# Kernel tuning notes

Measured on AMD Instinct MI355X. Metric: run time of the kernel, lower is better.

Reference implementation:

```python
import jax, jax.numpy as jnp
import numpy as np

N_NODES = 40000
N_EDGES = 640000
IN, HID, OUT = 128, 128, 47


def setup_inputs() -> dict:
    key = jax.random.key(0)
    ks = jax.random.split(key, 12)
    def glorot(k, shape):
        fan = sum(shape)
        return jax.random.normal(k, shape, dtype=jnp.float32) * jnp.sqrt(2.0 / fan)
    return {
        "x": jax.random.normal(ks[0], (N_NODES, IN), dtype=jnp.float32),
        "src": jax.random.randint(ks[1], (N_EDGES,), 0, N_NODES),
        "dst": jax.random.randint(ks[2], (N_EDGES,), 0, N_NODES),
        "W_self0": glorot(ks[3], (IN, HID)),
        "W_neigh0": glorot(ks[4], (IN, HID)),
        "b0": jnp.zeros((HID,), dtype=jnp.float32),
        "W_self1": glorot(ks[5], (HID, HID)),
        "W_neigh1": glorot(ks[6], (HID, HID)),
        "b1": jnp.zeros((HID,), dtype=jnp.float32),
        "W_self2": glorot(ks[7], (HID, OUT)),
        "W_neigh2": glorot(ks[8], (HID, OUT)),
        "b2": jnp.zeros((OUT,), dtype=jnp.float32),
    }


def _sage_conv(h, src, dst, W_self, W_neigh, b):
    # DGL SAGEConv('mean'): mean of neighbor (src) feats scattered to dst,
    # then fc_neigh(h_neigh) + fc_self(h_self) + bias.
    n = h.shape[0]
    deg = jax.ops.segment_sum(jnp.ones_like(dst, dtype=h.dtype), dst, num_segments=n)
    agg = jax.ops.segment_sum(h[src], dst, num_segments=n)          # [N, d] gather + scatter-add
    h_neigh = agg / jnp.maximum(deg, 1.0)[:, None]                   # isolated nodes -> 0 (DGL behavior)
    return h @ W_self + h_neigh @ W_neigh + b


def reference(x, src, dst, W_self0, W_neigh0, b0, W_self1, W_neigh1, b1,
              W_self2, W_neigh2, b2):
    # Dropout is identity in eval mode; omitted here.
    h = _sage_conv(x, src, dst, W_self0, W_neigh0, b0)
    h = jax.nn.relu(h)
    h = _sage_conv(h, src, dst, W_self1, W_neigh1, b1)
    h = jax.nn.relu(h)
    h = _sage_conv(h, src, dst, W_self2, W_neigh2, b2)
    return h
```

## Files before the change

kernel.cpp:

```cpp
#include <hip/hip_runtime.h>
#include <hip/hip_bf16.h>

#define NN 40000
#define NE 640000
#define NB 157

typedef __attribute__((ext_vector_type(8))) short bf16x8;
typedef __attribute__((ext_vector_type(4))) float f32x4;

static __device__ __forceinline__ unsigned short f2b(float f) {
    unsigned b = __float_as_uint(f);
    return (unsigned short)((b + 0x7FFFu + ((b >> 16) & 1u)) >> 16);
}
static __device__ __forceinline__ float blo(unsigned v) { return __uint_as_float(v << 16); }
static __device__ __forceinline__ float bhi(unsigned v) { return __uint_as_float(v & 0xffff0000u); }

static __device__ __forceinline__ void acc8(float* a, uint4 v) {
    a[0] += blo(v.x); a[1] += bhi(v.x);
    a[2] += blo(v.y); a[3] += bhi(v.y);
    a[4] += blo(v.z); a[5] += bhi(v.z);
    a[6] += blo(v.w); a[7] += bhi(v.w);
}
static __device__ __forceinline__ void acc4(float* a, uint2 v) {
    a[0] += blo(v.x); a[1] += bhi(v.x);
    a[2] += blo(v.y); a[3] += bhi(v.y);
}


__global__ void count_deg_kernel(const int* __restrict__ dst, int* __restrict__ deg, int n) {
    int i = blockIdx.x * blockDim.x + threadIdx.x;
    if (i < n) atomicAdd(&deg[dst[i]], 1);
}

__global__ __launch_bounds__(256) void scan1_kernel(const int* __restrict__ deg,
                                                    int* __restrict__ bsum) {
    int i = blockIdx.x * 256 + threadIdx.x;
    int v = (i < NN) ? deg[i] : 0;
#pragma unroll
    for (int off = 1; off < 64; off <<= 1) v += __shfl_xor(v, off);
    __shared__ int ws4[4];
    if ((threadIdx.x & 63) == 0) ws4[threadIdx.x >> 6] = v;
    __syncthreads();
    if (threadIdx.x == 0) bsum[blockIdx.x] = ws4[0] + ws4[1] + ws4[2] + ws4[3];
}

__global__ void scan_top_kernel(const int* __restrict__ bsum, int* __restrict__ btop) {
    int lane = threadIdx.x;
    int run = 0;
    for (int base = 0; base < NB; base += 64) {
        int idx = base + lane;
        int v = (idx < NB) ? bsum[idx] : 0;
        int s = v;
#pragma unroll
        for (int off = 1; off < 64; off <<= 1) { int t = __shfl_up(s, off); if (lane >= off) s += t; }
        if (idx < NB) btop[idx] = run + s - v;
        run += __shfl(s, 63);
    }
}

__global__ __launch_bounds__(256) void scan2_kernel(const int* __restrict__ deg,
                                                    const int* __restrict__ btop,
                                                    int* __restrict__ row_ptr) {
    int b = blockIdx.x;
    int i = b * 256 + threadIdx.x;
    int lane = threadIdx.x & 63, wv = threadIdx.x >> 6;
    int v = (i < NN) ? deg[i] : 0;
    int s = v;
#pragma unroll
    for (int off = 1; off < 64; off <<= 1) { int t = __shfl_up(s, off); if (lane >= off) s += t; }
    __shared__ int wsum[4];
    if (lane == 63) wsum[wv] = s;
    __syncthreads();
    int add = btop[b];
    for (int w = 0; w < wv; ++w) add += wsum[w];
    if (i < NN) row_ptr[i] = add + s - v;
    if (i == NN - 1) row_ptr[NN] = add + s;
}

__global__ void fill_csr_kernel(const int* __restrict__ src, const int* __restrict__ dst,
                                const int* __restrict__ row_ptr, int* __restrict__ cursor,
                                int* __restrict__ csr, int n) {
    int i = blockIdx.x * blockDim.x + threadIdx.x;
    if (i < n) {
        int d = dst[i];
        int pos = row_ptr[d] + atomicAdd(&cursor[d], 1);
        csr[pos] = src[i];
    }
}


__global__ __launch_bounds__(256) void prep_kernel(
    const float* __restrict__ x,
    const float* __restrict__ Ws0, const float* __restrict__ Wn0,
    const float* __restrict__ Ws1, const float* __restrict__ Wn1,
    const float* __restrict__ Ws2, const float* __restrict__ Wn2,
    int* __restrict__ zero_base, unsigned short* __restrict__ X,
    unsigned short* __restrict__ Wt0, unsigned short* __restrict__ Wt1,
    unsigned short* __restrict__ Wt2s, unsigned short* __restrict__ Wt2n) {
    int b = blockIdx.x, tid = threadIdx.x;
    if (b < 79) {
        int i = (b * 256 + tid) * 4;
        if (i < 80000) *(int4*)(zero_base + i) = (int4){0, 0, 0, 0};
    } else if (b < 5079) {
        int i = (b - 79) * 256 + tid;
        int e = i << 2;
        float4 v = *(const float4*)(x + e);
        uint2 o;
        o.x = f2b(v.x) | ((unsigned)f2b(v.y) << 16);
        o.y = f2b(v.z) | ((unsigned)f2b(v.w) << 16);
        *(uint2*)(X + e) = o;
    } else {
        int i = (b - 5079) * 256 + tid;
        if (i < 65536) {
            int l = i >> 15, j = i & 32767;
            int n = j >> 8, k = j & 255;
            const float* Ws = l ? Ws1 : Ws0;
            const float* Wn = l ? Wn1 : Wn0;
            float v = (k < 128) ? Ws[k * 128 + n] : Wn[(k - 128) * 128 + n];
            (l ? Wt1 : Wt0)[n * 256 + k] = f2b(v);
        } else if (i < 65536 + 6144) {
            int j = i - 65536;
            int n = j >> 7, k = j & 127;
            float v = (n < 47) ? Ws2[k * 47 + n] : 0.f;
            Wt2s[n * 128 + k] = f2b(v);
        } else if (i < 65536 + 12288) {
            int j = i - 65536 - 6144;
            int n = j >> 7, k = j & 127;
            float v = (n < 47) ? Wn2[k * 47 + n] : 0.f;
            Wt2n[n * 128 + k] = f2b(v);
        }
    }
}


template <bool RELU>
__global__ __launch_bounds__(256) void sage_layer_kernel(
    const unsigned short* __restrict__ Hin,
    const int* __restrict__ csr, const int* __restrict__ row_ptr,
    const unsigned short* __restrict__ Wt, const float* __restrict__ bias,
    unsigned short* __restrict__ Hout) {
    __shared__ unsigned short agg_lds[64 * 128];

    int tid = threadIdx.x;
    int wv = tid >> 6, lane = tid & 63;
    int lr = lane & 15, lg = lane >> 4;
    int m0 = blockIdx.x * 64;

    bf16x8 bfr[2][8];
    float bs[2];
#pragma unroll
    for (int c = 0; c < 2; ++c) {
        int n = (wv * 2 + c) * 16 + lr;
#pragma unroll
        for (int kt = 0; kt < 8; ++kt)
            bfr[c][kt] = *(const bf16x8*)(Wt + (size_t)n * 256 + kt * 32 + lg * 8);
        bs[c] = bias[n];
    }

    int nb = m0 + wv * 16;
    int rp = row_ptr[nb + (lane & 31) % 17];
    rp = __shfl(rp, lane % 17);
    int rp17 = (lane < 17) ? row_ptr[nb + lane] : 0;
    for (int t = 0; t < 16; ++t) {
        int beg = __shfl(rp17, t), end = __shfl(rp17, t + 1);
        float a[8] = {};
        int j = beg + lg;
        for (; j + 12 < end; j += 16) {
            int s0 = csr[j], s1 = csr[j + 4], s2 = csr[j + 8], s3 = csr[j + 12];
            uint4 v0 = *(const uint4*)(Hin + (size_t)s0 * 128 + lr * 8);
            uint4 v1 = *(const uint4*)(Hin + (size_t)s1 * 128 + lr * 8);
            uint4 v2 = *(const uint4*)(Hin + (size_t)s2 * 128 + lr * 8);
            uint4 v3 = *(const uint4*)(Hin + (size_t)s3 * 128 + lr * 8);
            acc8(a, v0); acc8(a, v1); acc8(a, v2); acc8(a, v3);
        }
        for (; j < end; j += 4) {
            uint4 v = *(const uint4*)(Hin + (size_t)csr[j] * 128 + lr * 8);
            acc8(a, v);
        }
#pragma unroll
        for (int k = 0; k < 8; ++k) {
            a[k] += __shfl_xor(a[k], 16);
            a[k] += __shfl_xor(a[k], 32);
        }
        if (lg == 0) {
            float inv = 1.0f / fmaxf((float)(end - beg), 1.0f);
            uint4 o;
            o.x = f2b(a[0] * inv) | ((unsigned)f2b(a[1] * inv) << 16);
            o.y = f2b(a[2] * inv) | ((unsigned)f2b(a[3] * inv) << 16);
            o.z = f2b(a[4] * inv) | ((unsigned)f2b(a[5] * inv) << 16);
            o.w = f2b(a[6] * inv) | ((unsigned)f2b(a[7] * inv) << 16);
            int row = wv * 16 + t;
            int chunk = lr ^ (row & 15);
            *(uint4*)&agg_lds[row * 128 + chunk * 8] = o;
        }
    }
    __syncthreads();

    for (int tt = 0; tt < 4; ++tt) {
        int mr = tt * 16 + lr;
        bf16x8 afr[8];
#pragma unroll
        for (int kt = 0; kt < 4; ++kt)
            afr[kt] = *(const bf16x8*)(Hin + (size_t)(m0 + mr) * 128 + kt * 32 + lg * 8);
#pragma unroll
        for (int kt = 0; kt < 4; ++kt) {
            int chunk = (kt * 4 + lg) ^ (mr & 15);
            afr[4 + kt] = *(const bf16x8*)&agg_lds[mr * 128 + chunk * 8];
        }
        f32x4 acc[2];
#pragma unroll
        for (int c = 0; c < 2; ++c) acc[c] = (f32x4){0.f, 0.f, 0.f, 0.f};
#pragma unroll
        for (int kt = 0; kt < 8; ++kt)
#pragma unroll
            for (int c = 0; c < 2; ++c)
                acc[c] = __builtin_amdgcn_mfma_f32_16x16x32_bf16(afr[kt], bfr[c][kt], acc[c], 0, 0, 0);
#pragma unroll
        for (int c = 0; c < 2; ++c) {
            int n = (wv * 2 + c) * 16 + lr;
#pragma unroll
            for (int r = 0; r < 4; ++r) {
                int m = m0 + tt * 16 + lg * 4 + r;
                float v = acc[c][r] + bs[c];
                if (RELU) v = fmaxf(v, 0.f);
                Hout[(size_t)m * 128 + n] = f2b(v);
            }
        }
    }
}


__global__ __launch_bounds__(192) void dual_gemm_kernel(
    const unsigned short* __restrict__ H2,
    const unsigned short* __restrict__ Wt2s, const unsigned short* __restrict__ Wt2n,
    const float* __restrict__ b2,
    float* __restrict__ out, unsigned short* __restrict__ Hn) {
    int wv = threadIdx.x >> 6, lane = threadIdx.x & 63;
    int lr = lane & 15, lg = lane >> 4;

    bf16x8 bfr[2][4];
    float bs[2];
#pragma unroll
    for (int c = 0; c < 2; ++c) {
        int t = wv * 2 + c;
        bool is_s = t < 3;
        int n = (is_s ? t : t - 3) * 16 + lr;
        const unsigned short* W = is_s ? Wt2s : Wt2n;
#pragma unroll
        for (int kt = 0; kt < 4; ++kt)
            bfr[c][kt] = *(const bf16x8*)(W + (size_t)n * 128 + kt * 32 + lg * 8);
        bs[c] = (is_s && n < 47) ? b2[n] : 0.f;
    }

    for (int tt = 0; tt < 4; ++tt) {
        int m0 = blockIdx.x * 64 + tt * 16;
        bf16x8 afr[4];
#pragma unroll
        for (int kt = 0; kt < 4; ++kt)
            afr[kt] = *(const bf16x8*)(H2 + (size_t)(m0 + lr) * 128 + kt * 32 + lg * 8);
        f32x4 acc[2];
#pragma unroll
        for (int c = 0; c < 2; ++c) acc[c] = (f32x4){0.f, 0.f, 0.f, 0.f};
#pragma unroll
        for (int kt = 0; kt < 4; ++kt)
#pragma unroll
            for (int c = 0; c < 2; ++c)
                acc[c] = __builtin_amdgcn_mfma_f32_16x16x32_bf16(afr[kt], bfr[c][kt], acc[c], 0, 0, 0);
#pragma unroll
        for (int c = 0; c < 2; ++c) {
            int t = wv * 2 + c;
            bool is_s = t < 3;
            int n = (is_s ? t : t - 3) * 16 + lr;
#pragma unroll
            for (int r = 0; r < 4; ++r) {
                int m = m0 + lg * 4 + r;
                float v = acc[c][r] + bs[c];
                if (is_s) {
                    if (n < 47) out[(size_t)m * 47 + n] = v;
                } else {
                    Hn[(size_t)m * 48 + n] = f2b(v);
                }
            }
        }
    }
}


__global__ void aggregate_out_kernel(const unsigned short* __restrict__ Hn,
                                     const int* __restrict__ csr,
                                     const int* __restrict__ row_ptr,
                                     float* __restrict__ out) {
    int node = (blockIdx.x * blockDim.x + threadIdx.x) >> 6;
    int lane = threadIdx.x & 63;
    if (node >= NN) return;
    int eg = lane >> 4, lc = lane & 15;
    int beg = row_ptr[node], end = row_ptr[node + 1];
    float a[4] = {};
    int j = beg + eg;
    for (; j + 12 < end; j += 16) {
        int s0 = csr[j], s1 = csr[j + 4], s2 = csr[j + 8], s3 = csr[j + 12];
        uint2 v0 = *(const uint2*)(Hn + (size_t)s0 * 48 + lc * 4);
        uint2 v1 = *(const uint2*)(Hn + (size_t)s1 * 48 + lc * 4);
        uint2 v2 = *(const uint2*)(Hn + (size_t)s2 * 48 + lc * 4);
        uint2 v3 = *(const uint2*)(Hn + (size_t)s3 * 48 + lc * 4);
        acc4(a, v0); acc4(a, v1); acc4(a, v2); acc4(a, v3);
    }
    for (; j < end; j += 4) {
        uint2 v = *(const uint2*)(Hn + (size_t)csr[j] * 48 + lc * 4);
        acc4(a, v);
    }
#pragma unroll
    for (int k = 0; k < 4; ++k) {
        a[k] += __shfl_xor(a[k], 16);
        a[k] += __shfl_xor(a[k], 32);
    }
    if (eg == 0 && lc < 12) {
        float inv = 1.0f / fmaxf((float)(end - beg), 1.0f);
        int c0 = lc * 4;
#pragma unroll
        for (int r = 0; r < 4; ++r)
            if (c0 + r < 47) out[(size_t)node * 47 + c0 + r] += a[r] * inv;
    }
}


extern "C" void kernel_launch(void* const* d_in, const int* in_sizes, int n_in,
                              void* d_out, int out_size, void* d_ws, size_t ws_size,
                              hipStream_t stream) {
    const float* x   = (const float*)d_in[0];
    const int*   src = (const int*)d_in[1];
    const int*   dst = (const int*)d_in[2];
    const float* Ws0 = (const float*)d_in[3];
    const float* Wn0 = (const float*)d_in[4];
    const float* b0  = (const float*)d_in[5];
    const float* Ws1 = (const float*)d_in[6];
    const float* Wn1 = (const float*)d_in[7];
    const float* b1  = (const float*)d_in[8];
    const float* Ws2 = (const float*)d_in[9];
    const float* Wn2 = (const float*)d_in[10];
    const float* b2  = (const float*)d_in[11];
    float* out = (float*)d_out;

    int* wsI     = (int*)d_ws;
    int* deg     = wsI;
    int* cursor  = wsI + 40000;
    int* row_ptr = wsI + 80000;
    int* csr     = wsI + 120004;
    unsigned short* X   = (unsigned short*)(wsI + 760004);
    unsigned short* H1  = X + (size_t)NN * 128;
    unsigned short* H2  = X;
    unsigned short* Wt0 = H1 + (size_t)NN * 128;
    unsigned short* Wt1 = Wt0 + 128 * 256;
    unsigned short* Wt2s = Wt1 + 128 * 256;
    unsigned short* Wt2n = Wt2s + 48 * 128;
    unsigned short* Hn  = Wt2n + 48 * 128;
    int* bsum = (int*)(Hn + (size_t)NN * 48 + 64);
    int* btop = bsum + NB;

    prep_kernel<<<5383, 256, 0, stream>>>(x, Ws0, Wn0, Ws1, Wn1, Ws2, Wn2,
                                          deg, X, Wt0, Wt1, Wt2s, Wt2n);
    count_deg_kernel<<<2500, 256, 0, stream>>>(dst, deg, NE);
    scan1_kernel<<<NB, 256, 0, stream>>>(deg, bsum);
    scan_top_kernel<<<1, 64, 0, stream>>>(bsum, btop);
    scan2_kernel<<<NB, 256, 0, stream>>>(deg, btop, row_ptr);
    fill_csr_kernel<<<2500, 256, 0, stream>>>(src, dst, row_ptr, cursor, csr, NE);

    sage_layer_kernel<true><<<625, 256, 0, stream>>>(X, csr, row_ptr, Wt0, b0, H1);
    sage_layer_kernel<true><<<625, 256, 0, stream>>>(H1, csr, row_ptr, Wt1, b1, H2);
    dual_gemm_kernel<<<625, 192, 0, stream>>>(H2, Wt2s, Wt2n, b2, out, Hn);
    aggregate_out_kernel<<<10000, 256, 0, stream>>>(Hn, csr, row_ptr, out);
}
```

Baseline: 216.4 us.

## Shrink per-block node tile to raise block count in SAGE layer kernels

Each block of the fused aggregate+GEMM layer kernel now handles 16 nodes instead of 64, so the launch grows from 625 to 2500 blocks. LDS use drops and weight fragments are loaded inside the MFMA loop instead of being held in registers. This aims to improve occupancy and load balance on the irregular gather phase, which had only 625 blocks for the GPU's many CUs. The cost is more redundant weight loads per node. The last-layer dual GEMM tile is also halved to give 1250 blocks.

```diff
diff --git a/kernel.cpp b/kernel.cpp
--- a/kernel.cpp
+++ b/kernel.cpp
@@ -139,30 +139,17 @@
     const int* __restrict__ csr, const int* __restrict__ row_ptr,
     const unsigned short* __restrict__ Wt, const float* __restrict__ bias,
     unsigned short* __restrict__ Hout) {
-    __shared__ unsigned short agg_lds[64 * 128];
+    __shared__ unsigned short agg_lds[16 * 128];
 
     int tid = threadIdx.x;
     int wv = tid >> 6, lane = tid & 63;
     int lr = lane & 15, lg = lane >> 4;
-    int m0 = blockIdx.x * 64;
-
-    bf16x8 bfr[2][8];
-    float bs[2];
-#pragma unroll
-    for (int c = 0; c < 2; ++c) {
-        int n = (wv * 2 + c) * 16 + lr;
-#pragma unroll
-        for (int kt = 0; kt < 8; ++kt)
-            bfr[c][kt] = *(const bf16x8*)(Wt + (size_t)n * 256 + kt * 32 + lg * 8);
-        bs[c] = bias[n];
-    }
-
-    int nb = m0 + wv * 16;
-    int rp = row_ptr[nb + (lane & 31) % 17];
-    rp = __shfl(rp, lane % 17);
-    int rp17 = (lane < 17) ? row_ptr[nb + lane] : 0;
-    for (int t = 0; t < 16; ++t) {
-        int beg = __shfl(rp17, t), end = __shfl(rp17, t + 1);
+    int m0 = blockIdx.x * 16;
+
+    int nb = m0 + wv * 4;
+    int rp5 = (lane < 5) ? row_ptr[nb + lane] : 0;
+    for (int t = 0; t < 4; ++t) {
+        int beg = __shfl(rp5, t), end = __shfl(rp5, t + 1);
         float a[8] = {};
         int j = beg + lg;
         for (; j + 12 < end; j += 16) {
@@ -189,43 +176,44 @@
             o.y = f2b(a[2] * inv) | ((unsigned)f2b(a[3] * inv) << 16);
             o.z = f2b(a[4] * inv) | ((unsigned)f2b(a[5] * inv) << 16);
             o.w = f2b(a[6] * inv) | ((unsigned)f2b(a[7] * inv) << 16);
-            int row = wv * 16 + t;
-            int chunk = lr ^ (row & 15);
+            int row = wv * 4 + t;
+            int chunk = lr ^ row;
             *(uint4*)&agg_lds[row * 128 + chunk * 8] = o;
         }
     }
     __syncthreads();
 
-    for (int tt = 0; tt < 4; ++tt) {
-        int mr = tt * 16 + lr;
-        bf16x8 afr[8];
-#pragma unroll
-        for (int kt = 0; kt < 4; ++kt)
-            afr[kt] = *(const bf16x8*)(Hin + (size_t)(m0 + mr) * 128 + kt * 32 + lg * 8);
-#pragma unroll
-        for (int kt = 0; kt < 4; ++kt) {
-            int chunk = (kt * 4 + lg) ^ (mr & 15);
-            afr[4 + kt] = *(const bf16x8*)&agg_lds[mr * 128 + chunk * 8];
-        }
-        f32x4 acc[2];
-#pragma unroll
-        for (int c = 0; c < 2; ++c) acc[c] = (f32x4){0.f, 0.f, 0.f, 0.f};
-#pragma unroll
-        for (int kt = 0; kt < 8; ++kt)
-#pragma unroll
-            for (int c = 0; c < 2; ++c)
-                acc[c] = __builtin_amdgcn_mfma_f32_16x16x32_bf16(afr[kt], bfr[c][kt], acc[c], 0, 0, 0);
-#pragma unroll
-        for (int c = 0; c < 2; ++c) {
-            int n = (wv * 2 + c) * 16 + lr;
-#pragma unroll
-            for (int r = 0; r < 4; ++r) {
-                int m = m0 + tt * 16 + lg * 4 + r;
-                float v = acc[c][r] + bs[c];
-                if (RELU) v = fmaxf(v, 0.f);
-                Hout[(size_t)m * 128 + n] = f2b(v);
-            }
-        }
+    bf16x8 afr[8];
+#pragma unroll
+    for (int kt = 0; kt < 4; ++kt)
+        afr[kt] = *(const bf16x8*)(Hin + (size_t)(m0 + lr) * 128 + kt * 32 + lg * 8);
+#pragma unroll
+    for (int kt = 0; kt < 4; ++kt) {
+        int chunk = (kt * 4 + lg) ^ lr;
+        afr[4 + kt] = *(const bf16x8*)&agg_lds[lr * 128 + chunk * 8];
+    }
+
+    int n0 = (wv * 2) * 16 + lr;
+    int n1 = n0 + 16;
+    f32x4 acc0 = (f32x4){0.f, 0.f, 0.f, 0.f};
+    f32x4 acc1 = (f32x4){0.f, 0.f, 0.f, 0.f};
+#pragma unroll
+    for (int kt = 0; kt < 8; ++kt) {
+        bf16x8 b0 = *(const bf16x8*)(Wt + (size_t)n0 * 256 + kt * 32 + lg * 8);
+        bf16x8 b1 = *(const bf16x8*)(Wt + (size_t)n1 * 256 + kt * 32 + lg * 8);
+        acc0 = __builtin_amdgcn_mfma_f32_16x16x32_bf16(afr[kt], b0, acc0, 0, 0, 0);
+        acc1 = __builtin_amdgcn_mfma_f32_16x16x32_bf16(afr[kt], b1, acc1, 0, 0, 0);
+    }
+
+    float bs0 = bias[n0], bs1 = bias[n1];
+#pragma unroll
+    for (int r = 0; r < 4; ++r) {
+        int m = m0 + lg * 4 + r;
+        float v0 = acc0[r] + bs0;
+        float v1 = acc1[r] + bs1;
+        if (RELU) { v0 = fmaxf(v0, 0.f); v1 = fmaxf(v1, 0.f); }
+        Hout[(size_t)m * 128 + n0] = f2b(v0);
+        Hout[(size_t)m * 128 + n1] = f2b(v1);
     }
 }
 
@@ -252,8 +240,8 @@
         bs[c] = (is_s && n < 47) ? b2[n] : 0.f;
     }
 
-    for (int tt = 0; tt < 4; ++tt) {
-        int m0 = blockIdx.x * 64 + tt * 16;
+    for (int tt = 0; tt < 2; ++tt) {
+        int m0 = blockIdx.x * 32 + tt * 16;
         bf16x8 afr[4];
 #pragma unroll
         for (int kt = 0; kt < 4; ++kt)
@@ -365,8 +353,8 @@
     scan2_kernel<<<NB, 256, 0, stream>>>(deg, btop, row_ptr);
     fill_csr_kernel<<<2500, 256, 0, stream>>>(src, dst, row_ptr, cursor, csr, NE);
 
-    sage_layer_kernel<true><<<625, 256, 0, stream>>>(X, csr, row_ptr, Wt0, b0, H1);
-    sage_layer_kernel<true><<<625, 256, 0, stream>>>(H1, csr, row_ptr, Wt1, b1, H2);
-    dual_gemm_kernel<<<625, 192, 0, stream>>>(H2, Wt2s, Wt2n, b2, out, Hn);
+    sage_layer_kernel<true><<<2500, 256, 0, stream>>>(X, csr, row_ptr, Wt0, b0, H1);
+    sage_layer_kernel<true><<<2500, 256, 0, stream>>>(H1, csr, row_ptr, Wt1, b1, H2);
+    dual_gemm_kernel<<<1250, 192, 0, stream>>>(H2, Wt2s, Wt2n, b2, out, Hn);
     aggregate_out_kernel<<<10000, 256, 0, stream>>>(Hn, csr, row_ptr, out);
 }
```

Measured after the change: 214.3 us. Within noise of the previous version (-1.0%).
